# Kernel optimization log

Measured on AMD Instinct MI355X. Metric: run time of the kernel, lower is better.

## Reference

```python
import jax, jax.numpy as jnp
import numpy as np

HEADS = 8
DIM_HEAD = 64
RMS_EPS = 1.1920929e-07  # torch default eps = finfo(fp32).eps


def rotate_half(x):
    x1, x2 = jnp.split(x, 2, axis=-1)
    return jnp.concatenate((-x2, x1), axis=-1)


def setup_inputs() -> dict:
    key = jax.random.key(0)
    k1, k2, k3, k4, k5 = jax.random.split(key, 5)
    b, n, dim = 2, 4096, 1024
    dim_hidden = HEADS * DIM_HEAD  # 512
    x = jax.random.normal(k1, (b, n, dim), dtype=jnp.float32)
    rotary_emb = jax.random.normal(k2, (n, DIM_HEAD), dtype=jnp.float32)
    rms_weight = jnp.ones((dim,), dtype=jnp.float32)
    w_qkv = jax.random.normal(k3, (dim, dim_hidden * 3), dtype=jnp.float32) * (dim ** -0.5)
    w_out = jax.random.normal(k4, (dim_hidden, dim), dtype=jnp.float32) * (dim_hidden ** -0.5)
    return {"x": x, "rotary_emb": rotary_emb, "rms_weight": rms_weight,
            "w_qkv": w_qkv, "w_out": w_out}


def reference(x, rotary_emb, rms_weight, w_qkv, w_out):
    b, n, dim = x.shape
    h, d = HEADS, DIM_HEAD
    # RMSNorm
    xn = x * jax.lax.rsqrt(jnp.mean(x * x, axis=-1, keepdims=True) + RMS_EPS) * rms_weight
    # QKV projection, rearrange 'b n (qkv h d) -> qkv b h n d'
    qkv = (xn @ w_qkv).reshape(b, n, 3, h, d).transpose(2, 0, 3, 1, 4)
    q, k, v = qkv[0], qkv[1], qkv[2]
    # RoPE
    cos, sin = jnp.cos(rotary_emb), jnp.sin(rotary_emb)  # (n, d) broadcasts over b,h
    q = q * cos + rotate_half(q) * sin
    k = k * cos + rotate_half(k) * sin
    q = q * (d ** -0.5)
    sim = jnp.einsum('bhid,bhjd->bhij', q, k)
    causal_mask = jnp.triu(jnp.ones((n, n), dtype=bool), 1)
    sim = jnp.where(causal_mask, -jnp.finfo(sim.dtype).max, sim)
    attn = jax.nn.softmax(sim, axis=-1)
    out = jnp.einsum('bhij,bhjd->bhid', attn, v)
    out = out.transpose(0, 2, 1, 3).reshape(b, n, h * d)  # 'b h n d -> b n (h d)'
    return out @ w_out
```

## Files before the change

### kernel.cpp

```cpp
#include <hip/hip_runtime.h>
#include <hip/hip_bf16.h>
#include <cstdint>

using bf16x8 = __attribute__((ext_vector_type(8))) __bf16;
using f32x4  = __attribute__((ext_vector_type(4))) float;

#define LOG2E 1.4426950408889634f

__device__ inline void gload16(__bf16* lds, const __bf16* g) {
    __builtin_amdgcn_global_load_lds((const __attribute__((address_space(1))) void*)g,
                                     (__attribute__((address_space(3))) void*)lds, 16, 0, 0);
}
__device__ inline void wait_barrier4() {
    asm volatile("s_waitcnt vmcnt(4)" ::: "memory");
    __builtin_amdgcn_s_barrier();
}
__device__ inline void wait_barrier0() {
    asm volatile("s_waitcnt vmcnt(0)" ::: "memory");
    __builtin_amdgcn_s_barrier();
}

__global__ __launch_bounds__(256) void rmsnorm_kernel(const float* __restrict__ x,
                                                      const float* __restrict__ w,
                                                      __bf16* __restrict__ xn) {
    const int row = blockIdx.x;
    const float4 v = reinterpret_cast<const float4*>(x + (size_t)row * 1024)[threadIdx.x];
    float ss = v.x * v.x + v.y * v.y + v.z * v.z + v.w * v.w;
#pragma unroll
    for (int i = 1; i < 64; i <<= 1) ss += __shfl_xor(ss, i);
    __shared__ float part[4];
    if ((threadIdx.x & 63) == 0) part[threadIdx.x >> 6] = ss;
    __syncthreads();
    const float total = part[0] + part[1] + part[2] + part[3];
    const float scale = rsqrtf(total * (1.0f / 1024.0f) + 1.1920929e-07f);
    const float4 wv = reinterpret_cast<const float4*>(w)[threadIdx.x];
    union { __bf16 h[4]; uint2 u; } pk;
    pk.h[0] = (__bf16)(v.x * scale * wv.x);
    pk.h[1] = (__bf16)(v.y * scale * wv.y);
    pk.h[2] = (__bf16)(v.z * scale * wv.z);
    pk.h[3] = (__bf16)(v.w * scale * wv.w);
    reinterpret_cast<uint2*>(xn + (size_t)row * 1024)[threadIdx.x] = pk.u;
}

__global__ void transpose_cast_kernel(const float* __restrict__ in,
                                      __bf16* __restrict__ out, int K, int N) {
    __shared__ float tile[32][33];
    const int n0 = blockIdx.x * 32, k0 = blockIdx.y * 32;
#pragma unroll
    for (int r = threadIdx.y; r < 32; r += 8)
        tile[r][threadIdx.x] = in[(size_t)(k0 + r) * N + n0 + threadIdx.x];
    __syncthreads();
#pragma unroll
    for (int r = threadIdx.y; r < 32; r += 8)
        out[(size_t)(n0 + r) * K + k0 + threadIdx.x] = (__bf16)tile[threadIdx.x][r];
}

__global__ __launch_bounds__(256) void csin_kernel(const float* __restrict__ rot,
                                                   float2* __restrict__ csin) {
    const int i = blockIdx.x * 256 + threadIdx.x;
    float s, c;
    sincosf(rot[i], &s, &c);
    csin[i] = make_float2(c, s);
}

__global__ __launch_bounds__(256) void rope_k_kernel(__bf16* __restrict__ qk,
                                                     const float2* __restrict__ csin) {
    const int row = blockIdx.x * 4 + (threadIdx.x >> 6);
    const int lane = threadIdx.x & 63;
    const int h = lane >> 3, dl = (lane & 7) * 4;
    const int pos = row & 4095;
    const float4 csA = *reinterpret_cast<const float4*>(&csin[pos * 64 + dl]);
    const float4 csB = *reinterpret_cast<const float4*>(&csin[pos * 64 + dl + 2]);
    const float4 csC = *reinterpret_cast<const float4*>(&csin[pos * 64 + dl + 32]);
    const float4 csD = *reinterpret_cast<const float4*>(&csin[pos * 64 + dl + 34]);
    const float c0[4] = {csA.x, csA.z, csB.x, csB.z};
    const float s0[4] = {csA.y, csA.w, csB.y, csB.w};
    const float c1[4] = {csC.x, csC.z, csD.x, csD.z};
    const float s1[4] = {csC.y, csC.w, csD.y, csD.w};
    __bf16* pp = qk + (size_t)row * 1024 + 512 + h * 64 + dl;
    union { uint2 u; __bf16 hh[4]; } va, vb, oa, ob;
    va.u = *reinterpret_cast<const uint2*>(pp);
    vb.u = *reinterpret_cast<const uint2*>(pp + 32);
#pragma unroll
    for (int j = 0; j < 4; ++j) {
        const float a = (float)va.hh[j], b2 = (float)vb.hh[j];
        oa.hh[j] = (__bf16)(a * c0[j] - b2 * s0[j]);
        ob.hh[j] = (__bf16)(b2 * c1[j] + a * s1[j]);
    }
    *reinterpret_cast<uint2*>(pp)      = oa.u;
    *reinterpret_cast<uint2*>(pp + 32) = ob.u;
}

template <typename OutT, int MODE>
__global__ __launch_bounds__(256) void gemm_bt(const __bf16* __restrict__ A,
                                               const __bf16* __restrict__ Bt,
                                               OutT* __restrict__ C,
                                               __bf16* __restrict__ vt,
                                               int M, int N, int K) {
    __shared__ __align__(16) __bf16 As[3][128 * 32];
    __shared__ __align__(16) __bf16 Bs[3][128 * 32];
    const int nbn = N >> 7;
    const int xcd = blockIdx.x & 7;
    const int idx = blockIdx.x >> 3;
    const int bm = xcd * 8 + idx / nbn;
    const int bn = idx % nbn;
    const int tid = threadIdx.x;
    const int w = tid >> 6, l = tid & 63, lg = l >> 4, lr = l & 15;
    const int wr = w >> 1, wc = w & 1;
    const __bf16* Ab = A + (size_t)(bm * 128) * K;
    const __bf16* Bb = Bt + (size_t)(bn * 128) * K;
    const int srow = tid >> 2, scol = (tid & 3) * 8;
    const __bf16* Asrc = Ab + (size_t)srow * K + scol;
    const __bf16* Bsrc = Bb + (size_t)srow * K + scol;

    auto stage = [&](int k2) {
        const int nx = k2 % 3;
        const int off = k2 * 32;
        gload16(&As[nx][tid * 8],        Asrc + off);
        gload16(&As[nx][2048 + tid * 8], Asrc + (size_t)64 * K + off);
        gload16(&Bs[nx][tid * 8],        Bsrc + off);
        gload16(&Bs[nx][2048 + tid * 8], Bsrc + (size_t)64 * K + off);
    };

    const int NS = K >> 5;
    f32x4 acc[4][4] = {};
    stage(0);
    stage(1);
    wait_barrier4();
    for (int k = 0; k < NS; ++k) {
        const bool more = (k + 2 < NS);
        if (more) stage(k + 2);
        const __bf16* Ac = &As[k % 3][0];
        const __bf16* Bc = &Bs[k % 3][0];
        bf16x8 af[4], bfr[4];
#pragma unroll
        for (int m = 0; m < 4; ++m)
            af[m] = *reinterpret_cast<const bf16x8*>(Ac + (wr * 64 + m * 16 + lr) * 32 + lg * 8);
#pragma unroll
        for (int nn = 0; nn < 4; ++nn)
            bfr[nn] = *reinterpret_cast<const bf16x8*>(Bc + (wc * 64 + nn * 16 + lr) * 32 + lg * 8);
#pragma unroll
        for (int m = 0; m < 4; ++m)
#pragma unroll
            for (int nn = 0; nn < 4; ++nn)
                acc[m][nn] = __builtin_amdgcn_mfma_f32_16x16x32_bf16(af[m], bfr[nn],
                                                                     acc[m][nn], 0, 0, 0);
        if (more) wait_barrier4();
        else      wait_barrier0();
    }
    if constexpr (MODE == 1) {
        const int cb = bn * 128 + wc * 64;
        if (cb < 1024) {
#pragma unroll
            for (int m = 0; m < 4; ++m) {
                const int rg = bm * 128 + wr * 64 + m * 16 + 4 * lg;
#pragma unroll
                for (int nn = 0; nn < 4; ++nn) {
                    const int cg = cb + nn * 16 + lr;
#pragma unroll
                    for (int r = 0; r < 4; ++r)
                        C[(size_t)(rg + r) * 1024 + cg] = (OutT)acc[m][nn][r];
                }
            }
        } else {
#pragma unroll
            for (int m = 0; m < 4; ++m) {
                const int rg = bm * 128 + wr * 64 + m * 16 + 4 * lg;
                const int bidx = rg >> 12, pos0 = rg & 4095;
                const int a0 = pos0 & 63;
                const int cp = 32 * (a0 >> 5) + 8 * ((a0 >> 2) & 3) + 4 * ((a0 >> 4) & 1);
                const int nbase = (pos0 & ~63) + cp;
#pragma unroll
                for (int nn = 0; nn < 4; ++nn) {
                    const int col = cb + nn * 16 + lr - 1024;
                    const int hh = col >> 6, dd = col & 63;
                    union { __bf16 h4[4]; uint2 u; } pk2;
#pragma unroll
                    for (int r = 0; r < 4; ++r) pk2.h4[r] = (__bf16)acc[m][nn][r];
                    *reinterpret_cast<uint2*>(&vt[((size_t)(bidx * 8 + hh) * 64 + dd) * 4096 + nbase]) = pk2.u;
                }
            }
        }
        return;
    }
#pragma unroll
    for (int m = 0; m < 4; ++m) {
        const int rg = bm * 128 + wr * 64 + m * 16 + 4 * lg;
#pragma unroll
        for (int nn = 0; nn < 4; ++nn) {
            const int cg = bn * 128 + wc * 64 + nn * 16 + lr;
#pragma unroll
            for (int r = 0; r < 4; ++r)
                C[(size_t)(rg + r) * N + cg] = (OutT)acc[m][nn][r];
        }
    }
}

__global__ __launch_bounds__(256) void attn_kernel(const __bf16* __restrict__ qkp,
                                                   const __bf16* __restrict__ vt,
                                                   const float2* __restrict__ csin,
                                                   __bf16* __restrict__ attn_out) {
    const int bid = blockIdx.x;
    const int j = bid >> 3;
    const int bh = 2 * (bid & 7) + (j & 1);
    const int qt = 63 - (j >> 1);
    const int b = bh >> 3, h = bh & 7;
    const int tid = threadIdx.x;
    const int w = tid >> 6, l = tid & 63, lg = l >> 4, lr = l & 15;

    __shared__ __align__(16) __bf16 Ks[2][64 * 64];
    __shared__ __align__(16) __bf16 Vs[3][64 * 64];

    const __bf16* qbase = qkp + (size_t)b * 4096 * 1024 + h * 64;
    const __bf16* kbase = qbase + 512;
    const __bf16* vtb   = vt + (size_t)(b * 8 + h) * 64 * 4096;

    const int sr = tid >> 3;
    const int sc = ((tid & 7) ^ (sr & 7)) * 8;
    const __bf16* kp = kbase + (size_t)sr * 1024 + sc;
    const __bf16* vp = vtb + (size_t)sr * 4096 + sc;

    const int xel = (lr & 7) * 8;

    const int wq0 = qt * 64 + 16 * w;
    const int nkt = qt + 1;

    auto stage2 = [&](__bf16* kdst, __bf16* vdst) {
        gload16(kdst + tid * 8,         kp);
        gload16(kdst + (tid + 256) * 8, kp + 32 * 1024);
        gload16(vdst + tid * 8,         vp);
        gload16(vdst + (tid + 256) * 8, vp + 32 * 4096);
        kp += 64 * 1024;
        vp += 64;
    };

    stage2(Ks[0], Vs[0]);
    stage2(Ks[1], Vs[1]);

    bf16x8 Qf[2];
    {
        const __bf16* qp = qbase + (size_t)(wq0 + lr) * 1024 + 8 * lg;
        const bf16x8 rq0 = *reinterpret_cast<const bf16x8*>(qp);
        const bf16x8 rq1 = *reinterpret_cast<const bf16x8*>(qp + 32);
        const float2* csp = csin + (size_t)(wq0 + lr) * 64 + 8 * lg;
        const float qs = 0.125f * LOG2E;
#pragma unroll
        for (int i = 0; i < 8; ++i) {
            const float2 ca = csp[i];
            const float2 cb = csp[i + 32];
            const float a = (float)rq0[i], b2 = (float)rq1[i];
            Qf[0][i] = (__bf16)((a * ca.x - b2 * ca.y) * qs);
            Qf[1][i] = (__bf16)((b2 * cb.x + a * cb.y) * qs);
        }
    }

    bf16x8 ones;
#pragma unroll
    for (int i = 0; i < 8; ++i) ones[i] = (__bf16)1.0f;

    f32x4 O[4] = {};
    f32x4 Lacc = {};
    float m_ = -1e30f;

    auto qk_step = [&](f32x4 (&S)[4], const __bf16* kb) {
        __builtin_amdgcn_s_setprio(1);
#pragma unroll
        for (int jt = 0; jt < 4; ++jt) {
            const __bf16* kr = kb + (16 * jt + lr) * 64;
            const bf16x8 Kf0 = *reinterpret_cast<const bf16x8*>(kr + ((8 * lg) ^ xel));
            const bf16x8 Kf1 = *reinterpret_cast<const bf16x8*>(kr + ((32 + 8 * lg) ^ xel));
            f32x4 z = {};
            z = __builtin_amdgcn_mfma_f32_16x16x32_bf16(Kf0, Qf[0], z, 0, 0, 0);
            S[jt] = __builtin_amdgcn_mfma_f32_16x16x32_bf16(Kf1, Qf[1], z, 0, 0, 0);
        }
        __builtin_amdgcn_s_setprio(0);
    };
    auto smpv = [&](f32x4 (&SC)[4], const __bf16* vb, bool domask) {
        if (domask) {
#pragma unroll
            for (int jt = 0; jt < 4; ++jt)
#pragma unroll
                for (int r = 0; r < 4; ++r)
                    if (16 * jt + 4 * lg + r > 16 * w + lr) SC[jt][r] = -1e30f;
        }
        float mx = -1e30f;
#pragma unroll
        for (int jt = 0; jt < 4; ++jt)
            mx = fmaxf(mx, fmaxf(fmaxf(SC[jt][0], SC[jt][1]), fmaxf(SC[jt][2], SC[jt][3])));
        if (__any(mx > m_ + 8.0f)) {
            mx = fmaxf(mx, __shfl_xor(mx, 16));
            mx = fmaxf(mx, __shfl_xor(mx, 32));
            const float mn = fmaxf(m_, mx);
            const float alpha = __builtin_amdgcn_exp2f(m_ - mn);
            m_ = mn;
            Lacc *= alpha;
#pragma unroll
            for (int dt = 0; dt < 4; ++dt) O[dt] *= alpha;
        }
#pragma unroll
        for (int jt = 0; jt < 4; ++jt)
#pragma unroll
            for (int r = 0; r < 4; ++r)
                SC[jt][r] = __builtin_amdgcn_exp2f(SC[jt][r] - m_);
        __builtin_amdgcn_s_setprio(1);
#pragma unroll
        for (int s = 0; s < 2; ++s) {
            bf16x8 Pf;
#pragma unroll
            for (int i = 0; i < 8; ++i)
                Pf[i] = (__bf16)SC[2 * s + (i >> 2)][i & 3];
            Lacc = __builtin_amdgcn_mfma_f32_16x16x32_bf16(ones, Pf, Lacc, 0, 0, 0);
#pragma unroll
            for (int dt = 0; dt < 4; ++dt) {
                const bf16x8 Vf = *reinterpret_cast<const bf16x8*>(
                    vb + (16 * dt + lr) * 64 + ((32 * s + 8 * lg) ^ xel));
                O[dt] = __builtin_amdgcn_mfma_f32_16x16x32_bf16(Vf, Pf, O[dt], 0, 0, 0);
            }
        }
        __builtin_amdgcn_s_setprio(0);
    };

    f32x4 S0[4], S1[4];
    int t = 0;

    __syncthreads();
    qk_step(S0, Ks[0]);
    __syncthreads();

    for (; t + 8 <= nkt; t += 6) {
        stage2(Ks[0], Vs[2]); qk_step(S1, Ks[1]); smpv(S0, Vs[0], false); __syncthreads();
        stage2(Ks[1], Vs[0]); qk_step(S0, Ks[0]); smpv(S1, Vs[1], false); __syncthreads();
        stage2(Ks[0], Vs[1]); qk_step(S1, Ks[1]); smpv(S0, Vs[2], false); __syncthreads();
        stage2(Ks[1], Vs[2]); qk_step(S0, Ks[0]); smpv(S1, Vs[0], false); __syncthreads();
        stage2(Ks[0], Vs[0]); qk_step(S1, Ks[1]); smpv(S0, Vs[1], false); __syncthreads();
        stage2(Ks[1], Vs[1]); qk_step(S0, Ks[0]); smpv(S1, Vs[2], false); __syncthreads();
    }

    {
        f32x4 Sp[4];
#pragma unroll
        for (int jt = 0; jt < 4; ++jt) Sp[jt] = S0[jt];
        for (; t < nkt; ++t) {
            if (t + 2 < nkt) stage2(Ks[(t + 2) & 1], Vs[(t + 2) % 3]);
            f32x4 Sn[4];
            if (t + 1 < nkt) qk_step(Sn, Ks[(t + 1) & 1]);
            smpv(Sp, Vs[t % 3], t == nkt - 1);
            __syncthreads();
#pragma unroll
            for (int jt = 0; jt < 4; ++jt) Sp[jt] = Sn[jt];
        }
    }

    const float inv = 1.0f / Lacc[0];
    __bf16* op = attn_out + ((size_t)b * 4096 + wq0 + lr) * 512 + h * 64;
#pragma unroll
    for (int dt = 0; dt < 4; ++dt) {
        union { __bf16 h4[4]; uint2 u; } ow;
#pragma unroll
        for (int r = 0; r < 4; ++r) ow.h4[r] = (__bf16)(O[dt][r] * inv);
        *reinterpret_cast<uint2*>(op + 16 * dt + 4 * lg) = ow.u;
    }
}

extern "C" void kernel_launch(void* const* d_in, const int* in_sizes, int n_in,
                              void* d_out, int out_size, void* d_ws, size_t ws_size,
                              hipStream_t stream) {
    (void)in_sizes; (void)n_in; (void)out_size; (void)ws_size;
    const float* x    = (const float*)d_in[0];
    const float* rot  = (const float*)d_in[1];
    const float* rmsw = (const float*)d_in[2];
    const float* wqkv = (const float*)d_in[3];
    const float* wout = (const float*)d_in[4];
    float* out = (float*)d_out;

    char* ws = (char*)d_ws;
    __bf16* xn    = (__bf16*)ws;
    __bf16* wqkvt = (__bf16*)(ws + 16777216);
    __bf16* woutt = (__bf16*)(ws + 16777216 + 3145728);
    __bf16* aout  = (__bf16*)(ws + 16777216 + 3145728 + 1048576);
    __bf16* qk   = (__bf16*)d_out;
    float2* csin = (float2*)((char*)d_out + 16777216);
    __bf16* vt   = (__bf16*)((char*)d_out + 18874368);

    rmsnorm_kernel<<<8192, 256, 0, stream>>>(x, rmsw, xn);
    transpose_cast_kernel<<<dim3(48, 32), dim3(32, 8), 0, stream>>>(wqkv, wqkvt, 1024, 1536);
    transpose_cast_kernel<<<dim3(32, 16), dim3(32, 8), 0, stream>>>(wout, woutt, 512, 1024);
    csin_kernel<<<1024, 256, 0, stream>>>(rot, csin);
    gemm_bt<__bf16, 1><<<768, 256, 0, stream>>>(xn, wqkvt, qk, vt, 8192, 1536, 1024);
    rope_k_kernel<<<2048, 256, 0, stream>>>(qk, csin);
    attn_kernel<<<1024, 256, 0, stream>>>(qk, vt, csin, aout);
    gemm_bt<float, 0><<<512, 256, 0, stream>>>(aout, woutt, out, nullptr, 8192, 1024, 512);
}
```

Measured before the change: 136.7 us.

## Double the attention query tile per block to reuse K/V loads across rows

Each attention block now processes 128 query rows (32 per wave, two 16-row subtiles) instead of 64, so every staged K/V tile feeds twice as many MFMAs and total K/V traffic is halved. The grid drops to 512 blocks with a new block-to-(batch,head,qtile) mapping that pairs short and long causal tiles per XCD. K gets a third LDS buffer so the extra sync after the first QK step can be removed, and per-subtile masking and skipping handle the causal tail. Register pressure roughly doubles for the O/S accumulators, which may reduce occupancy, and fewer blocks could hurt load balance.

```diff
diff --git a/kernel.cpp b/kernel.cpp
--- a/kernel.cpp
+++ b/kernel.cpp
@@ -201,14 +201,16 @@
                                                    const float2* __restrict__ csin,
                                                    __bf16* __restrict__ attn_out) {
     const int bid = blockIdx.x;
+    const int xcd = bid & 7;
     const int j = bid >> 3;
-    const int bh = 2 * (bid & 7) + (j & 1);
-    const int qt = 63 - (j >> 1);
+    const int hs = j >> 5;
+    const int qt = hs ? (j - 32) : (31 - j);
+    const int bh = 2 * xcd + hs;
     const int b = bh >> 3, h = bh & 7;
     const int tid = threadIdx.x;
     const int w = tid >> 6, l = tid & 63, lg = l >> 4, lr = l & 15;
 
-    __shared__ __align__(16) __bf16 Ks[2][64 * 64];
+    __shared__ __align__(16) __bf16 Ks[3][64 * 64];
     __shared__ __align__(16) __bf16 Vs[3][64 * 64];
 
     const __bf16* qbase = qkp + (size_t)b * 4096 * 1024 + h * 64;
@@ -222,8 +224,8 @@
 
     const int xel = (lr & 7) * 8;
 
-    const int wq0 = qt * 64 + 16 * w;
-    const int nkt = qt + 1;
+    const int wq0 = qt * 128 + 32 * w;
+    const int nkt = 2 * qt + 2;
 
     auto stage2 = [&](__bf16* kdst, __bf16* vdst) {
         gload16(kdst + tid * 8,         kp);
@@ -237,20 +239,22 @@
     stage2(Ks[0], Vs[0]);
     stage2(Ks[1], Vs[1]);
 
-    bf16x8 Qf[2];
-    {
-        const __bf16* qp = qbase + (size_t)(wq0 + lr) * 1024 + 8 * lg;
+    bf16x8 Qf[2][2];
+#pragma unroll
+    for (int nt = 0; nt < 2; ++nt) {
+        const int qrow = wq0 + 16 * nt + lr;
+        const __bf16* qp = qbase + (size_t)qrow * 1024 + 8 * lg;
         const bf16x8 rq0 = *reinterpret_cast<const bf16x8*>(qp);
         const bf16x8 rq1 = *reinterpret_cast<const bf16x8*>(qp + 32);
-        const float2* csp = csin + (size_t)(wq0 + lr) * 64 + 8 * lg;
+        const float2* csp = csin + (size_t)qrow * 64 + 8 * lg;
         const float qs = 0.125f * LOG2E;
 #pragma unroll
         for (int i = 0; i < 8; ++i) {
             const float2 ca = csp[i];
             const float2 cb = csp[i + 32];
             const float a = (float)rq0[i], b2 = (float)rq1[i];
-            Qf[0][i] = (__bf16)((a * ca.x - b2 * ca.y) * qs);
-            Qf[1][i] = (__bf16)((b2 * cb.x + a * cb.y) * qs);
+            Qf[nt][0][i] = (__bf16)((a * ca.x - b2 * ca.y) * qs);
+            Qf[nt][1][i] = (__bf16)((b2 * cb.x + a * cb.y) * qs);
         }
     }
 
@@ -258,107 +262,139 @@
 #pragma unroll
     for (int i = 0; i < 8; ++i) ones[i] = (__bf16)1.0f;
 
-    f32x4 O[4] = {};
-    f32x4 Lacc = {};
-    float m_ = -1e30f;
-
-    auto qk_step = [&](f32x4 (&S)[4], const __bf16* kb) {
+    f32x4 O[2][4] = {};
+    f32x4 Lacc[2] = {};
+    float m_[2] = {-1e30f, -1e30f};
+
+    auto qk_step = [&](f32x4 (&S)[2][4], const __bf16* kb) {
         __builtin_amdgcn_s_setprio(1);
 #pragma unroll
         for (int jt = 0; jt < 4; ++jt) {
             const __bf16* kr = kb + (16 * jt + lr) * 64;
             const bf16x8 Kf0 = *reinterpret_cast<const bf16x8*>(kr + ((8 * lg) ^ xel));
             const bf16x8 Kf1 = *reinterpret_cast<const bf16x8*>(kr + ((32 + 8 * lg) ^ xel));
-            f32x4 z = {};
-            z = __builtin_amdgcn_mfma_f32_16x16x32_bf16(Kf0, Qf[0], z, 0, 0, 0);
-            S[jt] = __builtin_amdgcn_mfma_f32_16x16x32_bf16(Kf1, Qf[1], z, 0, 0, 0);
+#pragma unroll
+            for (int nt = 0; nt < 2; ++nt) {
+                f32x4 z = {};
+                z = __builtin_amdgcn_mfma_f32_16x16x32_bf16(Kf0, Qf[nt][0], z, 0, 0, 0);
+                S[nt][jt] = __builtin_amdgcn_mfma_f32_16x16x32_bf16(Kf1, Qf[nt][1], z, 0, 0, 0);
+            }
         }
         __builtin_amdgcn_s_setprio(0);
     };
-    auto smpv = [&](f32x4 (&SC)[4], const __bf16* vb, bool domask) {
-        if (domask) {
+    auto smpv = [&](f32x4 (&SC)[2][4], const __bf16* vb, int kt0, bool tail) {
+        bool act[2] = {true, true};
+        if (tail) {
+#pragma unroll
+            for (int nt = 0; nt < 2; ++nt) {
+                act[nt] = (64 * kt0 <= wq0 + 16 * nt + 15);
+                if (act[nt] && 64 * kt0 + 63 > wq0 + 16 * nt) {
+                    const int thr = wq0 + 16 * nt + lr - 64 * kt0;
+#pragma unroll
+                    for (int jt = 0; jt < 4; ++jt)
+#pragma unroll
+                        for (int r = 0; r < 4; ++r)
+                            if (16 * jt + 4 * lg + r > thr) SC[nt][jt][r] = -1e30f;
+                }
+            }
+        }
+#pragma unroll
+        for (int nt = 0; nt < 2; ++nt) {
+            if (!act[nt]) continue;
+            float mx = -1e30f;
 #pragma unroll
             for (int jt = 0; jt < 4; ++jt)
+                mx = fmaxf(mx, fmaxf(fmaxf(SC[nt][jt][0], SC[nt][jt][1]),
+                                     fmaxf(SC[nt][jt][2], SC[nt][jt][3])));
+            if (__any(mx > m_[nt] + 8.0f)) {
+                mx = fmaxf(mx, __shfl_xor(mx, 16));
+                mx = fmaxf(mx, __shfl_xor(mx, 32));
+                const float mn = fmaxf(m_[nt], mx);
+                const float alpha = __builtin_amdgcn_exp2f(m_[nt] - mn);
+                m_[nt] = mn;
+                Lacc[nt] *= alpha;
+#pragma unroll
+                for (int dt = 0; dt < 4; ++dt) O[nt][dt] *= alpha;
+            }
+#pragma unroll
+            for (int jt = 0; jt < 4; ++jt)
 #pragma unroll
                 for (int r = 0; r < 4; ++r)
-                    if (16 * jt + 4 * lg + r > 16 * w + lr) SC[jt][r] = -1e30f;
-        }
-        float mx = -1e30f;
-#pragma unroll
-        for (int jt = 0; jt < 4; ++jt)
-            mx = fmaxf(mx, fmaxf(fmaxf(SC[jt][0], SC[jt][1]), fmaxf(SC[jt][2], SC[jt][3])));
-        if (__any(mx > m_ + 8.0f)) {
-            mx = fmaxf(mx, __shfl_xor(mx, 16));
-            mx = fmaxf(mx, __shfl_xor(mx, 32));
-            const float mn = fmaxf(m_, mx);
-            const float alpha = __builtin_amdgcn_exp2f(m_ - mn);
-            m_ = mn;
-            Lacc *= alpha;
-#pragma unroll
-            for (int dt = 0; dt < 4; ++dt) O[dt] *= alpha;
-        }
-#pragma unroll
-        for (int jt = 0; jt < 4; ++jt)
-#pragma unroll
-            for (int r = 0; r < 4; ++r)
-                SC[jt][r] = __builtin_amdgcn_exp2f(SC[jt][r] - m_);
+                    SC[nt][jt][r] = __builtin_amdgcn_exp2f(SC[nt][jt][r] - m_[nt]);
+        }
+        bf16x8 Pf[2][2];
+#pragma unroll
+        for (int nt = 0; nt < 2; ++nt)
+            if (act[nt])
+#pragma unroll
+                for (int s = 0; s < 2; ++s)
+#pragma unroll
+                    for (int i = 0; i < 8; ++i)
+                        Pf[nt][s][i] = (__bf16)SC[nt][2 * s + (i >> 2)][i & 3];
         __builtin_amdgcn_s_setprio(1);
 #pragma unroll
-        for (int s = 0; s < 2; ++s) {
-            bf16x8 Pf;
-#pragma unroll
-            for (int i = 0; i < 8; ++i)
-                Pf[i] = (__bf16)SC[2 * s + (i >> 2)][i & 3];
-            Lacc = __builtin_amdgcn_mfma_f32_16x16x32_bf16(ones, Pf, Lacc, 0, 0, 0);
+        for (int nt = 0; nt < 2; ++nt)
+            if (act[nt])
+#pragma unroll
+                for (int s = 0; s < 2; ++s)
+                    Lacc[nt] = __builtin_amdgcn_mfma_f32_16x16x32_bf16(ones, Pf[nt][s], Lacc[nt], 0, 0, 0);
+#pragma unroll
+        for (int s = 0; s < 2; ++s)
 #pragma unroll
             for (int dt = 0; dt < 4; ++dt) {
                 const bf16x8 Vf = *reinterpret_cast<const bf16x8*>(
                     vb + (16 * dt + lr) * 64 + ((32 * s + 8 * lg) ^ xel));
-                O[dt] = __builtin_amdgcn_mfma_f32_16x16x32_bf16(Vf, Pf, O[dt], 0, 0, 0);
-            }
-        }
+                if (act[0]) O[0][dt] = __builtin_amdgcn_mfma_f32_16x16x32_bf16(Vf, Pf[0][s], O[0][dt], 0, 0, 0);
+                if (act[1]) O[1][dt] = __builtin_amdgcn_mfma_f32_16x16x32_bf16(Vf, Pf[1][s], O[1][dt], 0, 0, 0);
+            }
         __builtin_amdgcn_s_setprio(0);
     };
 
-    f32x4 S0[4], S1[4];
+    f32x4 S0[2][4], S1[2][4];
     int t = 0;
 
     __syncthreads();
     qk_step(S0, Ks[0]);
-    __syncthreads();
 
     for (; t + 8 <= nkt; t += 6) {
-        stage2(Ks[0], Vs[2]); qk_step(S1, Ks[1]); smpv(S0, Vs[0], false); __syncthreads();
-        stage2(Ks[1], Vs[0]); qk_step(S0, Ks[0]); smpv(S1, Vs[1], false); __syncthreads();
-        stage2(Ks[0], Vs[1]); qk_step(S1, Ks[1]); smpv(S0, Vs[2], false); __syncthreads();
-        stage2(Ks[1], Vs[2]); qk_step(S0, Ks[0]); smpv(S1, Vs[0], false); __syncthreads();
-        stage2(Ks[0], Vs[0]); qk_step(S1, Ks[1]); smpv(S0, Vs[1], false); __syncthreads();
-        stage2(Ks[1], Vs[1]); qk_step(S0, Ks[0]); smpv(S1, Vs[2], false); __syncthreads();
+        stage2(Ks[2], Vs[2]); qk_step(S1, Ks[1]); smpv(S0, Vs[0], t,     false); __syncthreads();
+        stage2(Ks[0], Vs[0]); qk_step(S0, Ks[2]); smpv(S1, Vs[1], t + 1, false); __syncthreads();
+        stage2(Ks[1], Vs[1]); qk_step(S1, Ks[0]); smpv(S0, Vs[2], t + 2, false); __syncthreads();
+        stage2(Ks[2], Vs[2]); qk_step(S0, Ks[1]); smpv(S1, Vs[0], t + 3, false); __syncthreads();
+        stage2(Ks[0], Vs[0]); qk_step(S1, Ks[2]); smpv(S0, Vs[1], t + 4, false); __syncthreads();
+        stage2(Ks[1], Vs[1]); qk_step(S0, Ks[0]); smpv(S1, Vs[2], t + 5, false); __syncthreads();
     }
 
     {
-        f32x4 Sp[4];
-#pragma unroll
-        for (int jt = 0; jt < 4; ++jt) Sp[jt] = S0[jt];
+        f32x4 Sp[2][4];
+#pragma unroll
+        for (int nt = 0; nt < 2; ++nt)
+#pragma unroll
+            for (int jt = 0; jt < 4; ++jt) Sp[nt][jt] = S0[nt][jt];
         for (; t < nkt; ++t) {
-            if (t + 2 < nkt) stage2(Ks[(t + 2) & 1], Vs[(t + 2) % 3]);
-            f32x4 Sn[4];
-            if (t + 1 < nkt) qk_step(Sn, Ks[(t + 1) & 1]);
-            smpv(Sp, Vs[t % 3], t == nkt - 1);
+            if (t + 2 < nkt) stage2(Ks[(t + 2) % 3], Vs[(t + 2) % 3]);
+            f32x4 Sn[2][4];
+            if (t + 1 < nkt) qk_step(Sn, Ks[(t + 1) % 3]);
+            smpv(Sp, Vs[t % 3], t, true);
             __syncthreads();
 #pragma unroll
-            for (int jt = 0; jt < 4; ++jt) Sp[jt] = Sn[jt];
-        }
-    }
-
-    const float inv = 1.0f / Lacc[0];
-    __bf16* op = attn_out + ((size_t)b * 4096 + wq0 + lr) * 512 + h * 64;
-#pragma unroll
-    for (int dt = 0; dt < 4; ++dt) {
-        union { __bf16 h4[4]; uint2 u; } ow;
-#pragma unroll
-        for (int r = 0; r < 4; ++r) ow.h4[r] = (__bf16)(O[dt][r] * inv);
-        *reinterpret_cast<uint2*>(op + 16 * dt + 4 * lg) = ow.u;
+            for (int nt = 0; nt < 2; ++nt)
+#pragma unroll
+                for (int jt = 0; jt < 4; ++jt) Sp[nt][jt] = Sn[nt][jt];
+        }
+    }
+
+#pragma unroll
+    for (int nt = 0; nt < 2; ++nt) {
+        const float inv = 1.0f / Lacc[nt][0];
+        __bf16* op = attn_out + ((size_t)b * 4096 + wq0 + 16 * nt + lr) * 512 + h * 64;
+#pragma unroll
+        for (int dt = 0; dt < 4; ++dt) {
+            union { __bf16 h4[4]; uint2 u; } ow;
+#pragma unroll
+            for (int r = 0; r < 4; ++r) ow.h4[r] = (__bf16)(O[nt][dt][r] * inv);
+            *reinterpret_cast<uint2*>(op + 16 * dt + 4 * lg) = ow.u;
+        }
     }
 }
 
@@ -388,6 +424,6 @@
     csin_kernel<<<1024, 256, 0, stream>>>(rot, csin);
     gemm_bt<__bf16, 1><<<768, 256, 0, stream>>>(xn, wqkvt, qk, vt, 8192, 1536, 1024);
     rope_k_kernel<<<2048, 256, 0, stream>>>(qk, csin);
-    attn_kernel<<<1024, 256, 0, stream>>>(qk, vt, csin, aout);
+    attn_kernel<<<512, 256, 0, stream>>>(qk, vt, csin, aout);
     gemm_bt<float, 0><<<512, 256, 0, stream>>>(aout, woutt, out, nullptr, 8192, 1024, 512);
 }
```

New measurement: 197.5 us. 1.44x slower.

## Replace QKV GEMM with 256x256-tile 8-wave kernel using swizzled LDS pipeline

Applied to the files above, without the earlier changes.

The QKV projection moves from a 128x128-tile, 4-wave GEMM to a dedicated 256x256-tile kernel with 512 threads and 8 waves. It double-buffers 64-wide K slices in LDS with an XOR swizzle to avoid bank conflicts, and interleaves async global-to-LDS loads with MFMA groups under s_setprio. The larger tiles cut operand reloads from global memory and raise MFMA density per load. In exchange the grid shrinks to 192 blocks, which is under one wave of blocks for the CU count and may leave CUs idle, and the kernel carries higher register and LDS pressure.

```diff
diff --git a/kernel.cpp b/kernel.cpp
--- a/kernel.cpp
+++ b/kernel.cpp
@@ -18,6 +18,13 @@
 __device__ inline void wait_barrier0() {
     asm volatile("s_waitcnt vmcnt(0)" ::: "memory");
     __builtin_amdgcn_s_barrier();
+}
+__device__ inline void bar_mem() {
+    asm volatile("s_barrier" ::: "memory");
+}
+__device__ inline void vm_bar(int n) {
+    if (n == 0) asm volatile("s_waitcnt vmcnt(0)\ns_barrier" ::: "memory");
+    else        asm volatile("s_waitcnt vmcnt(4)\ns_barrier" ::: "memory");
 }
 
 __global__ __launch_bounds__(256) void rmsnorm_kernel(const float* __restrict__ x,
@@ -91,12 +98,142 @@
     *reinterpret_cast<uint2*>(pp + 32) = ob.u;
 }
 
-template <typename OutT, int MODE>
-__global__ __launch_bounds__(256) void gemm_bt(const __bf16* __restrict__ A,
-                                               const __bf16* __restrict__ Bt,
-                                               OutT* __restrict__ C,
-                                               __bf16* __restrict__ vt,
-                                               int M, int N, int K) {
+__global__ __launch_bounds__(512) void gemm8_qkv(const __bf16* __restrict__ A,
+                                                 const __bf16* __restrict__ Bt,
+                                                 __bf16* __restrict__ qk,
+                                                 __bf16* __restrict__ vt) {
+    __shared__ __align__(16) __bf16 AL[2 * 2 * 8192];
+    __shared__ __align__(16) __bf16 BL[2 * 2 * 8192];
+    const int xcd = blockIdx.x & 7;
+    const int idx = blockIdx.x >> 3;
+    const int bm = xcd * 4 + idx / 6;
+    const int bn = idx % 6;
+    const int tid = threadIdx.x;
+    const int wid = tid >> 6, l = tid & 63, lg = l >> 4, lr = l & 15;
+    const int wr = wid >> 2, wc = wid & 3;
+    const int swzr = (lr >> 1) & 3;
+
+    const int srow0 = tid >> 2;
+    const int sswz = (tid & 3) ^ ((srow0 >> 1) & 3);
+    const __bf16* Asrc0 = A + (size_t)(bm * 256 + srow0) * 1024 + sswz * 8;
+    const __bf16* Asrc1 = Asrc0 + (size_t)128 * 1024;
+    const __bf16* Bsrc0 = Bt + (size_t)(bn * 256 + srow0) * 1024 + sswz * 8;
+    const __bf16* Bsrc1 = Bsrc0 + (size_t)128 * 1024;
+
+    auto stageA = [&](int buf, int kk, int t) {
+        __bf16* base = AL + buf * 16384 + kk * 8192;
+        gload16(base + tid * 8,        Asrc0 + t * 64 + kk * 32);
+        gload16(base + 4096 + tid * 8, Asrc1 + t * 64 + kk * 32);
+    };
+    auto stageB = [&](int buf, int kk, int t) {
+        __bf16* base = BL + buf * 16384 + kk * 8192;
+        gload16(base + tid * 8,        Bsrc0 + t * 64 + kk * 32);
+        gload16(base + 4096 + tid * 8, Bsrc1 + t * 64 + kk * 32);
+    };
+
+    f32x4 acc[8][4] = {};
+    bf16x8 bcache[4];
+
+    auto loadA = [&](bf16x8 (&af)[4], int buf, int kk, int rh) {
+        const __bf16* base = AL + buf * 16384 + kk * 8192;
+#pragma unroll
+        for (int mm = 0; mm < 4; ++mm) {
+            const int row = wr * 128 + (4 * rh + mm) * 16 + lr;
+            af[mm] = *reinterpret_cast<const bf16x8*>(base + row * 32 + ((lg ^ swzr) << 3));
+        }
+    };
+    auto loadB = [&](int buf, int kk) {
+        const __bf16* base = BL + buf * 16384 + kk * 8192;
+#pragma unroll
+        for (int nn = 0; nn < 4; ++nn) {
+            const int row = wc * 64 + nn * 16 + lr;
+            bcache[nn] = *reinterpret_cast<const bf16x8*>(base + row * 32 + ((lg ^ swzr) << 3));
+        }
+    };
+    auto mfma16 = [&](bf16x8 (&af)[4], int rh) {
+        __builtin_amdgcn_s_setprio(1);
+#pragma unroll
+        for (int mm = 0; mm < 4; ++mm)
+#pragma unroll
+            for (int nn = 0; nn < 4; ++nn)
+                acc[4 * rh + mm][nn] = __builtin_amdgcn_mfma_f32_16x16x32_bf16(
+                    af[mm], bcache[nn], acc[4 * rh + mm][nn], 0, 0, 0);
+        __builtin_amdgcn_s_setprio(0);
+    };
+
+    stageA(0, 0, 0); stageB(0, 0, 0);
+    stageA(0, 1, 0); stageB(0, 1, 0);
+    stageA(1, 0, 1); stageB(1, 0, 1);
+    vm_bar(4);
+
+    const int NITER = 8;
+    for (int I = 0; I < NITER; ++I) {
+        const bool more = (I < NITER - 1);
+        bf16x8 af[4];
+        loadA(af, 0, 0, 0); loadB(0, 0);
+        stageA(1, 1, 2 * I + 1); stageB(1, 1, 2 * I + 1);
+        bar_mem(); mfma16(af, 0); bar_mem();
+        loadA(af, 0, 0, 1);
+        bar_mem(); mfma16(af, 1); bar_mem();
+        loadA(af, 0, 1, 0); loadB(0, 1);
+        if (more) stageA(0, 0, 2 * I + 2);
+        bar_mem(); mfma16(af, 0); bar_mem();
+        loadA(af, 0, 1, 1);
+        if (more) { stageB(0, 0, 2 * I + 2); vm_bar(4); }
+        else      { vm_bar(0); }
+        mfma16(af, 1); bar_mem();
+        loadA(af, 1, 0, 0); loadB(1, 0);
+        if (more) { stageA(0, 1, 2 * I + 2); stageB(0, 1, 2 * I + 2); }
+        bar_mem(); mfma16(af, 0); bar_mem();
+        loadA(af, 1, 0, 1);
+        bar_mem(); mfma16(af, 1); bar_mem();
+        loadA(af, 1, 1, 0); loadB(1, 1);
+        if (more) stageA(1, 0, 2 * I + 3);
+        bar_mem(); mfma16(af, 0); bar_mem();
+        loadA(af, 1, 1, 1);
+        if (more) { stageB(1, 0, 2 * I + 3); vm_bar(4); }
+        else      { vm_bar(0); }
+        mfma16(af, 1); bar_mem();
+    }
+
+    const int cb = bn * 256 + wc * 64;
+    if (cb < 1024) {
+#pragma unroll
+        for (int m = 0; m < 8; ++m) {
+            const int rg = bm * 256 + wr * 128 + m * 16 + 4 * lg;
+#pragma unroll
+            for (int nn = 0; nn < 4; ++nn) {
+                const int cg = cb + nn * 16 + lr;
+#pragma unroll
+                for (int r = 0; r < 4; ++r)
+                    qk[(size_t)(rg + r) * 1024 + cg] = (__bf16)acc[m][nn][r];
+            }
+        }
+    } else {
+#pragma unroll
+        for (int m = 0; m < 8; ++m) {
+            const int rg = bm * 256 + wr * 128 + m * 16 + 4 * lg;
+            const int bidx = rg >> 12, pos0 = rg & 4095;
+            const int a0 = pos0 & 63;
+            const int cp = 32 * (a0 >> 5) + 8 * ((a0 >> 2) & 3) + 4 * ((a0 >> 4) & 1);
+            const int nbase = (pos0 & ~63) + cp;
+#pragma unroll
+            for (int nn = 0; nn < 4; ++nn) {
+                const int col = cb + nn * 16 + lr - 1024;
+                const int hh = col >> 6, dd = col & 63;
+                union { __bf16 h4[4]; uint2 u; } pk2;
+#pragma unroll
+                for (int r = 0; r < 4; ++r) pk2.h4[r] = (__bf16)acc[m][nn][r];
+                *reinterpret_cast<uint2*>(&vt[((size_t)(bidx * 8 + hh) * 64 + dd) * 4096 + nbase]) = pk2.u;
+            }
+        }
+    }
+}
+
+__global__ __launch_bounds__(256) void gemm_out(const __bf16* __restrict__ A,
+                                                const __bf16* __restrict__ Bt,
+                                                float* __restrict__ C,
+                                                int M, int N, int K) {
     __shared__ __align__(16) __bf16 As[3][128 * 32];
     __shared__ __align__(16) __bf16 Bs[3][128 * 32];
     const int nbn = N >> 7;
@@ -148,41 +285,6 @@
         if (more) wait_barrier4();
         else      wait_barrier0();
     }
-    if constexpr (MODE == 1) {
-        const int cb = bn * 128 + wc * 64;
-        if (cb < 1024) {
-#pragma unroll
-            for (int m = 0; m < 4; ++m) {
-                const int rg = bm * 128 + wr * 64 + m * 16 + 4 * lg;
-#pragma unroll
-                for (int nn = 0; nn < 4; ++nn) {
-                    const int cg = cb + nn * 16 + lr;
-#pragma unroll
-                    for (int r = 0; r < 4; ++r)
-                        C[(size_t)(rg + r) * 1024 + cg] = (OutT)acc[m][nn][r];
-                }
-            }
-        } else {
-#pragma unroll
-            for (int m = 0; m < 4; ++m) {
-                const int rg = bm * 128 + wr * 64 + m * 16 + 4 * lg;
-                const int bidx = rg >> 12, pos0 = rg & 4095;
-                const int a0 = pos0 & 63;
-                const int cp = 32 * (a0 >> 5) + 8 * ((a0 >> 2) & 3) + 4 * ((a0 >> 4) & 1);
-                const int nbase = (pos0 & ~63) + cp;
-#pragma unroll
-                for (int nn = 0; nn < 4; ++nn) {
-                    const int col = cb + nn * 16 + lr - 1024;
-                    const int hh = col >> 6, dd = col & 63;
-                    union { __bf16 h4[4]; uint2 u; } pk2;
-#pragma unroll
-                    for (int r = 0; r < 4; ++r) pk2.h4[r] = (__bf16)acc[m][nn][r];
-                    *reinterpret_cast<uint2*>(&vt[((size_t)(bidx * 8 + hh) * 64 + dd) * 4096 + nbase]) = pk2.u;
-                }
-            }
-        }
-        return;
-    }
 #pragma unroll
     for (int m = 0; m < 4; ++m) {
         const int rg = bm * 128 + wr * 64 + m * 16 + 4 * lg;
@@ -191,7 +293,7 @@
             const int cg = bn * 128 + wc * 64 + nn * 16 + lr;
 #pragma unroll
             for (int r = 0; r < 4; ++r)
-                C[(size_t)(rg + r) * N + cg] = (OutT)acc[m][nn][r];
+                C[(size_t)(rg + r) * N + cg] = acc[m][nn][r];
         }
     }
 }
@@ -386,8 +488,8 @@
     transpose_cast_kernel<<<dim3(48, 32), dim3(32, 8), 0, stream>>>(wqkv, wqkvt, 1024, 1536);
     transpose_cast_kernel<<<dim3(32, 16), dim3(32, 8), 0, stream>>>(wout, woutt, 512, 1024);
     csin_kernel<<<1024, 256, 0, stream>>>(rot, csin);
-    gemm_bt<__bf16, 1><<<768, 256, 0, stream>>>(xn, wqkvt, qk, vt, 8192, 1536, 1024);
+    gemm8_qkv<<<192, 512, 0, stream>>>(xn, wqkvt, qk, vt);
     rope_k_kernel<<<2048, 256, 0, stream>>>(qk, csin);
     attn_kernel<<<1024, 256, 0, stream>>>(qk, vt, csin, aout);
-    gemm_bt<float, 0><<<512, 256, 0, stream>>>(aout, woutt, out, nullptr, 8192, 1024, 512);
-}
+    gemm_out<<<512, 256, 0, stream>>>(aout, woutt, out, 8192, 1024, 512);
+}
```

Result: no change. 137.0 us (+0.2%).
